# Performance work log

Hardware: AMD Instinct MI355X
Metric: run time of the kernel (lower is better)

## Reference

```python
import jax, jax.numpy as jnp
import numpy as np

B, S, I, C, N, V, O = 32, 256, 256, 512, 1024, 64, 256
EPS = 1e-12


def setup_inputs() -> dict:
    key = jax.random.key(0)
    ks = iter(jax.random.split(key, 40))

    def rn(shape, scale=0.05):
        return (jax.random.normal(next(ks), shape, jnp.float32) * scale)

    inp = {
        'x': jax.random.normal(next(ks), (B, S, I), jnp.float32),
        # LSTM controller (PyTorch gate order i,f,g,o)
        'lstm_Wih': rn((4 * C, I + V)), 'lstm_Whh': rn((4 * C, C)),
        'lstm_bih': rn((4 * C,)), 'lstm_bhh': rn((4 * C,)),
        # read head
        'r_key_W': rn((V, C)), 'r_key_b': rn((V,)),
        'r_str_W': rn((1, C)), 'r_str_b': rn((1,)),
        'r_gate_W': rn((1, C)), 'r_gate_b': rn((1,)),
        'r_shift_W': rn((3, C)), 'r_shift_b': rn((3,)),
        'r_gamma_W': rn((1, C)), 'r_gamma_b': rn((1,)),
        # write head (uses its own key/strength layers, plus erase/add)
        'w_key_W': rn((V, C)), 'w_key_b': rn((V,)),
        'w_str_W': rn((1, C)), 'w_str_b': rn((1,)),
        'w_erase_W': rn((V, C)), 'w_erase_b': rn((V,)),
        'w_add_W': rn((V, C)), 'w_add_b': rn((V,)),
        # output projection
        'out_W': rn((O, C + V)), 'out_b': rn((O,)),
    }
    return inp


def _lin(x, W, b):
    return x @ W.T + b


def _normalize(x, axis):
    n = jnp.linalg.norm(x, axis=axis, keepdims=True)
    return x / jnp.maximum(n, EPS)


def _content_addressing(key_vec, memory, strength):
    # key_vec: [B,V], memory: [B,N,V], strength: [B,1]
    kn = _normalize(key_vec, 1)
    mn = _normalize(memory, 2)
    sim = jnp.einsum('bv,bnv->bn', kn, mn)
    return jax.nn.softmax(strength * sim, axis=1)


def _ntm_forward(x, lstm_Wih, lstm_Whh, lstm_bih, lstm_bhh,
                 r_key_W, r_key_b, r_str_W, r_str_b, r_gate_W, r_gate_b,
                 r_shift_W, r_shift_b, r_gamma_W, r_gamma_b,
                 w_key_W, w_key_b, w_str_W, w_str_b,
                 w_erase_W, w_erase_b, w_add_W, w_add_b, out_W, out_b):
    b = x.shape[0]
    h0 = jnp.zeros((b, C), x.dtype)
    c0 = jnp.zeros((b, C), x.dtype)
    mem0 = jnp.zeros((b, N, V), x.dtype)
    rv0 = jnp.zeros((b, V), x.dtype)

    def step(carry, xt):
        h, c, memory, read_vec = carry
        # LSTM cell
        ci = jnp.concatenate([xt, read_vec], axis=1)          # [B, I+V]
        gates = _lin(ci, lstm_Wih, lstm_bih) + _lin(h, lstm_Whh, lstm_bhh)
        ig, fg, gg, og = jnp.split(gates, 4, axis=1)
        c = jax.nn.sigmoid(fg) * c + jax.nn.sigmoid(ig) * jnp.tanh(gg)
        h = jax.nn.sigmoid(og) * jnp.tanh(c)

        # read head
        key_r = jnp.tanh(_lin(h, r_key_W, r_key_b))
        str_r = jax.nn.softplus(_lin(h, r_str_W, r_str_b))
        gate = jax.nn.sigmoid(_lin(h, r_gate_W, r_gate_b))
        _shift = jax.nn.softmax(_lin(h, r_shift_W, r_shift_b), axis=1)  # computed but unused (as in source)
        gamma = 1.0 + jax.nn.softplus(_lin(h, r_gamma_W, r_gamma_b))
        cw = _content_addressing(key_r, memory, str_r)        # [B,N]
        sharp = cw ** gamma
        lw = sharp / jnp.sum(sharp, axis=1, keepdims=True)
        fw = gate * lw + (1.0 - gate) * cw
        read_vec = jnp.einsum('bn,bnv->bv', fw, memory)

        # write head (erase then add)
        key_w = jnp.tanh(_lin(h, w_key_W, w_key_b))
        str_w = jax.nn.softplus(_lin(h, w_str_W, w_str_b))
        ww = _content_addressing(key_w, memory, str_w)        # [B,N]
        erase = jax.nn.sigmoid(_lin(h, w_erase_W, w_erase_b))  # [B,V]
        add = jnp.tanh(_lin(h, w_add_W, w_add_b))              # [B,V]
        memory = memory * (1.0 - ww[:, :, None] * erase[:, None, :]) \
                 + ww[:, :, None] * add[:, None, :]

        out = _lin(jnp.concatenate([h, read_vec], axis=1), out_W, out_b)
        return (h, c, memory, read_vec), out

    (_, _, final_memory, _), outs = jax.lax.scan(
        step, (h0, c0, mem0, rv0), jnp.swapaxes(x, 0, 1))
    return jnp.swapaxes(outs, 0, 1), final_memory


def reference(x, lstm_Wih, lstm_Whh, lstm_bih, lstm_bhh,
              r_key_W, r_key_b, r_str_W, r_str_b, r_gate_W, r_gate_b,
              r_shift_W, r_shift_b, r_gamma_W, r_gamma_b,
              w_key_W, w_key_b, w_str_W, w_str_b,
              w_erase_W, w_erase_b, w_add_W, w_add_b, out_W, out_b):
    return _ntm_forward(x, lstm_Wih, lstm_Whh, lstm_bih, lstm_bhh,
                        r_key_W, r_key_b, r_str_W, r_str_b, r_gate_W, r_gate_b,
                        r_shift_W, r_shift_b, r_gamma_W, r_gamma_b,
                        w_key_W, w_key_b, w_str_W, w_str_b,
                        w_erase_W, w_erase_b, w_add_W, w_add_b, out_W, out_b)
```

## Files before the change

kernel.cpp:

```cpp
#include <hip/hip_runtime.h>

#define Bv 32
#define Sv 256
#define Iv 256
#define Cv 512
#define Nv 1024
#define Vv 64
#define Ov 256
#define NBLK 256
#define NTHR 256

#define CLAIM_I(x)   ((x)*8)
#define GAL_I(x,q)   (64 + ((x)*4+(q))*8)
#define XROOT_I(x)   (320 + (x)*8)
#define ZERO_BYTES   (640*4)
#define FBASE 1024
#define HBU(x,t1,bb)  (FBASE + (x)*2048 + (t1)*1024 + (bb)*256)
#define EGU(x,bb,k)   (FBASE + 16384 + (x)*2048 + (bb)*512 + (k)*64)
#define SUMPF(x,bb,k) (FBASE + 32768 + (x)*128 + (bb)*32 + (k)*4)
#define HPF(x,bb,r)   (FBASE + 33792 + (((x)*4+(bb))*32 + (r))*264)

struct KP {
  const float *x, *Wih, *Whh, *bih, *bhh;
  const float *rkW, *rkb, *rsW, *rsb, *rgW, *rgb, *rgammaW, *rgammab;
  const float *wkW, *wkb, *wsW, *wsb, *weW, *web, *waW, *wab;
  const float *outW, *outb;
  float *out;
  float *memout;
  float *ws;
};

typedef _Float16 half2v __attribute__((ext_vector_type(2)));
union HU { unsigned u; half2v h; };

__device__ inline float sigf(float x){ return 1.f/(1.f+expf(-x)); }
__device__ inline float softplusf(float x){ return fmaxf(x,0.f) + log1pf(expf(-fabsf(x))); }
__device__ inline unsigned packh(float a, float b){
  HU z; z.h = half2v{(_Float16)a, (_Float16)b}; return z.u;
}
__device__ inline float h2lo(unsigned u){ HU z; z.u = u; return (float)z.h.x; }
__device__ inline float h2hi(unsigned u){ HU z; z.u = u; return (float)z.h.y; }
__device__ inline float dot2(unsigned w, unsigned a, float acc){
  HU wu, au; wu.u = w; au.u = a;
  return __builtin_amdgcn_fdot2(wu.h, au.h, acc, false);
}

__device__ inline void stg_f(float* p, float v){
  asm volatile("global_store_dword %0, %1, off sc0" :: "v"(p), "v"(v) : "memory");
}
__device__ inline void stg_u(unsigned* p, unsigned v){
  asm volatile("global_store_dword %0, %1, off sc0" :: "v"(p), "v"(v) : "memory");
}
#define LDG4U(dst, addr) asm volatile("global_load_dwordx4 %0, %1, off sc0" : "=v"(dst) : "v"(addr) : "memory")
#define LDG4F(dst, addr) asm volatile("global_load_dwordx4 %0, %1, off sc0" : "=v"(dst) : "v"(addr) : "memory")
#define LDGU(dst, addr)  asm volatile("global_load_dword %0, %1, off sc0"  : "=v"(dst) : "v"(addr) : "memory")
#define LDGF(dst, addr)  asm volatile("global_load_dword %0, %1, off sc0"  : "=v"(dst) : "v"(addr) : "memory")
#define WAITV do { asm volatile("s_waitcnt vmcnt(0)" ::: "memory"); __builtin_amdgcn_sched_barrier(0); } while(0)

#define AADD(p,v) __hip_atomic_fetch_add((p),(v),__ATOMIC_RELAXED,__HIP_MEMORY_SCOPE_AGENT)
#define ALD(p)    __hip_atomic_load((p),__ATOMIC_RELAXED,__HIP_MEMORY_SCOPE_AGENT)

#define SPIN(cond_expr) do { unsigned sp = 0; \
  while (cond_expr){ __builtin_amdgcn_s_sleep(2); \
    if (((++sp)&1023u)==0u && (__builtin_amdgcn_s_memrealtime()-t0) > 300000000ULL) break; } } while(0)

__device__ inline float headact(int o, float s){
  if (o < 64)  return tanhf(s);
  if (o == 64) return softplusf(s);
  if (o == 65) return sigf(s);
  if (o == 66) return 1.f + softplusf(s);
  if (o < 131) return tanhf(s);
  if (o == 131) return softplusf(s);
  if (o < 196) return sigf(s);
  return tanhf(s);
}
__device__ inline void head_src(const KP& P, int o, const float** row, float* bias){
  if (o < 64)       { *row = P.rkW + o*Cv;        *bias = P.rkb[o]; }
  else if (o == 64) { *row = P.rsW;               *bias = P.rsb[0]; }
  else if (o == 65) { *row = P.rgW;               *bias = P.rgb[0]; }
  else if (o == 66) { *row = P.rgammaW;           *bias = P.rgammab[0]; }
  else if (o < 131) { *row = P.wkW + (o-67)*Cv;   *bias = P.wkb[o-67]; }
  else if (o == 131){ *row = P.wsW;               *bias = P.wsb[0]; }
  else if (o < 196) { *row = P.weW + (o-132)*Cv;  *bias = P.web[o-132]; }
  else              { *row = P.waW + (o-196)*Cv;  *bias = P.wab[o-196]; }
}

__global__ __launch_bounds__(NTHR) void ntm_kernel(KP P){
  __shared__ unsigned actL[4][420];
  __shared__ float memL[128][66];
  __shared__ float gbq[4][4][68];
  __shared__ float biasL[64];
  __shared__ float htmpf[16][5];
  __shared__ float headsL[264];
  __shared__ float pendE[64], pendA[64];
  __shared__ float knr[64], knw[64];
  __shared__ float scal[8];
  __shared__ float erL2[128], egL2[128], ewL[128];
  __shared__ float red[32][9];
  __shared__ float red2[2][4];
  __shared__ float sumS1[4][8][4];
  __shared__ float cEL[4], cGL[4];
  __shared__ float rvpE[4][64], rvpG[4][64];
  __shared__ float rvfinE[64], rvfinG[64];
  __shared__ int sXcd, sRank;

  const int tid = threadIdx.x;
  float* wsf = P.ws;
  unsigned* wsu = (unsigned*)P.ws;
  int* wsi = (int*)P.ws;
  const unsigned long long t0 = __builtin_amdgcn_s_memrealtime();

  if (tid == 0){
    unsigned xcc;
    asm volatile("s_getreg_b32 %0, hwreg(20, 0, 32)" : "=s"(xcc));
    int xc = (int)(xcc & 7u);
    int rk = AADD(&wsi[CLAIM_I(xc)], 1);
    sXcd = xc; sRank = rk & 31;
  }
  __syncthreads();
  const int xcd = sXcd, rank = sRank;
  const int bl_own = rank >> 3;
  const int rk8 = rank & 7;
  const int bglob = xcd*4 + bl_own;

  const int qw = tid >> 6;
  const int rw = tid & 63;
  const int grw = (rw>>4)*Cv + rank*16 + (rw&15);
  uint4 wreg[26];
  {
    #pragma unroll
    for (int jj = 0; jj < 26; ++jj){
      unsigned uu[4];
      #pragma unroll
      for (int c = 0; c < 4; ++c){
        int e = qw*208 + 8*jj + 2*c;
        float2 w2;
        if (e < 320) w2 = *(const float2*)(P.Wih + grw*320 + e);
        else         w2 = *(const float2*)(P.Whh + grw*512 + (e-320));
        uu[c] = packh(w2.x, w2.y);
      }
      wreg[jj].x = uu[0]; wreg[jj].y = uu[1]; wreg[jj].z = uu[2]; wreg[jj].w = uu[3];
    }
  }
  if (tid < 64){
    int gr = (tid>>4)*Cv + rank*16 + (tid&15);
    biasL[tid] = P.bih[gr] + P.bhh[gr];
  }
  float wA[16], wB[16], bA = 0.f, bB = 0.f;
  {
    const float* rowA; head_src(P, tid, &rowA, &bA);
    #pragma unroll
    for (int j = 0; j < 16; ++j) wA[j] = rowA[rank*16 + j];
    const float* rowB; head_src(P, 256 + (tid & 3), &rowB, &bB);
    #pragma unroll
    for (int j = 0; j < 16; ++j) wB[j] = rowB[rank*16 + j];
  }
  for (int idx = tid; idx < 128*66; idx += NTHR) ((float*)memL)[idx] = 0.f;
  __syncthreads();

  float cS = 0.f;
  int gs = 0;
  const int sbb = tid>>6, spart = tid&63;
  float4 xv;
  uint4 hq = {};
  xv = *(const float4*)(P.x + ((size_t)(xcd*4+sbb)*Sv + 0)*Iv + spart*4);

  for (int t = 0; t < Sv; ++t){
    if (t > 0){
      unsigned e0,e1,e2,e3,e4,e5,e6,e7,g0,g1,g2,g3,g4,g5,g6,g7;
      float4 sv = {0,0,0,0};
      int b2 = tid>>5, j = tid&31;
      if (tid < 128){
        const unsigned* eb = wsu + EGU(xcd,b2,0) + j;
        LDGU(e0,eb+0*64); LDGU(e1,eb+1*64); LDGU(e2,eb+2*64); LDGU(e3,eb+3*64);
        LDGU(e4,eb+4*64); LDGU(e5,eb+5*64); LDGU(e6,eb+6*64); LDGU(e7,eb+7*64);
        const unsigned* ggb = eb + 32;
        LDGU(g0,ggb+0*64); LDGU(g1,ggb+1*64); LDGU(g2,ggb+2*64); LDGU(g3,ggb+3*64);
        LDGU(g4,ggb+4*64); LDGU(g5,ggb+5*64); LDGU(g6,ggb+6*64); LDGU(g7,ggb+7*64);
      }
      if (tid < 32){ LDG4F(sv, wsf + SUMPF(xcd, tid>>3, tid&7)); }
      WAITV;
      actL[sbb][spart*2]   = packh(xv.x, xv.y);
      actL[sbb][spart*2+1] = packh(xv.z, xv.w);
      *(uint4*)&actL[sbb][160 + spart*4] = hq;
      if (tid < 32) *(float4*)&sumS1[tid>>3][tid&7][0] = sv;
      __syncthreads();
      if (tid < 4){
        float Se = 0.f, Sg = 0.f;
        #pragma unroll
        for (int k2 = 0; k2 < 8; ++k2){ Se += sumS1[tid][k2][0]; Sg += sumS1[tid][k2][1]; }
        float g = sumS1[tid][0][3];
        cEL[tid] = (1.f - g)/Se;
        cGL[tid] = g/Sg;
      }
      if (tid == 0){
        float Sw = 0.f;
        #pragma unroll
        for (int k2 = 0; k2 < 8; ++k2) Sw += sumS1[0][k2][2] + sumS1[1][k2][2] + sumS1[2][k2][2] + sumS1[3][k2][2];
        scal[6] = 0.f;
      }
      __syncthreads();
      if (tid == 0){
        float Sw = 0.f;
        #pragma unroll
        for (int k2 = 0; k2 < 8; ++k2) Sw += sumS1[bl_own][k2][2];
        scal[6] = Sw;
      }
      if (tid < 128){
        float Elo = h2lo(e0)+h2lo(e1)+h2lo(e2)+h2lo(e3)+h2lo(e4)+h2lo(e5)+h2lo(e6)+h2lo(e7);
        float Ehi = h2hi(e0)+h2hi(e1)+h2hi(e2)+h2hi(e3)+h2hi(e4)+h2hi(e5)+h2hi(e6)+h2hi(e7);
        float Glo = h2lo(g0)+h2lo(g1)+h2lo(g2)+h2lo(g3)+h2lo(g4)+h2lo(g5)+h2lo(g6)+h2lo(g7);
        float Ghi = h2hi(g0)+h2hi(g1)+h2hi(g2)+h2hi(g3)+h2hi(g4)+h2hi(g5)+h2hi(g6)+h2hi(g7);
        actL[b2][128 + j] = packh(cGL[b2]*Glo + cEL[b2]*Elo, cGL[b2]*Ghi + cEL[b2]*Ehi);
      }
      __syncthreads();
      {
        float rSw = 1.f/scal[6];
        #pragma unroll 4
        for (int e9 = 0; e9 < 32; ++e9){
          int flat = tid + e9*256;
          int r = flat >> 6, v2 = flat & 63;
          float ww = ewL[r]*rSw;
          memL[r][v2] = memL[r][v2]*(1.f - ww*pendE[v2]) + ww*pendA[v2];
        }
      }
    } else {
      actL[sbb][spart*2]   = packh(xv.x, xv.y);
      actL[sbb][spart*2+1] = packh(xv.z, xv.w);
      for (int idx = tid; idx < 4*288; idx += NTHR){
        int bb2 = idx/288, u = 128 + idx%288;
        actL[bb2][u] = 0u;
      }
    }
    __syncthreads();
    {
      const int base0 = qw*104;
      float a00=0.f,a01=0.f,a10=0.f,a11=0.f,a20=0.f,a21=0.f,a30=0.f,a31=0.f;
      #pragma unroll
      for (int jj = 0; jj < 26; ++jj){
        uint4 w = wreg[jj];
        uint4 v0 = *(const uint4*)&actL[0][base0+4*jj];
        uint4 v1 = *(const uint4*)&actL[1][base0+4*jj];
        uint4 v2 = *(const uint4*)&actL[2][base0+4*jj];
        uint4 v3 = *(const uint4*)&actL[3][base0+4*jj];
        a00=dot2(w.x,v0.x,a00); a01=dot2(w.y,v0.y,a01); a00=dot2(w.z,v0.z,a00); a01=dot2(w.w,v0.w,a01);
        a10=dot2(w.x,v1.x,a10); a11=dot2(w.y,v1.y,a11); a10=dot2(w.z,v1.z,a10); a11=dot2(w.w,v1.w,a11);
        a20=dot2(w.x,v2.x,a20); a21=dot2(w.y,v2.y,a21); a20=dot2(w.z,v2.z,a20); a21=dot2(w.w,v2.w,a21);
        a30=dot2(w.x,v3.x,a30); a31=dot2(w.y,v3.y,a31); a30=dot2(w.z,v3.z,a30); a31=dot2(w.w,v3.w,a31);
      }
      gbq[qw][0][rw] = a00+a01;
      gbq[qw][1][rw] = a10+a11;
      gbq[qw][2][rw] = a20+a21;
      gbq[qw][3][rw] = a30+a31;
    }
    __syncthreads();
    if (tid < 64){
      int j = tid>>2, bb = tid&3;
      float ig = biasL[j]    + gbq[0][bb][j]    + gbq[1][bb][j]    + gbq[2][bb][j]    + gbq[3][bb][j];
      float fg = biasL[16+j] + gbq[0][bb][16+j] + gbq[1][bb][16+j] + gbq[2][bb][16+j] + gbq[3][bb][16+j];
      float gg = biasL[32+j] + gbq[0][bb][32+j] + gbq[1][bb][32+j] + gbq[2][bb][32+j] + gbq[3][bb][32+j];
      float og = biasL[48+j] + gbq[0][bb][48+j] + gbq[1][bb][48+j] + gbq[2][bb][48+j] + gbq[3][bb][48+j];
      cS = sigf(fg)*cS + sigf(ig)*tanhf(gg);
      htmpf[j][bb] = sigf(og)*tanhf(cS);
    }
    __syncthreads();
    if (tid < 32){
      int pr = tid>>2, bb = tid&3;
      stg_u(wsu + HBU(xcd,t&1,bb) + rank*8 + pr, packh(htmpf[2*pr][bb], htmpf[2*pr+1][bb]));
    }
    {
      float p0=0.f,p1=0.f,p2=0.f,p3=0.f,q0=0.f,q1=0.f,q2=0.f,q3=0.f;
      #pragma unroll
      for (int j = 0; j < 16; ++j){
        float h0=htmpf[j][0], h1=htmpf[j][1], h2=htmpf[j][2], h3=htmpf[j][3];
        p0+=wA[j]*h0; p1+=wA[j]*h1; p2+=wA[j]*h2; p3+=wA[j]*h3;
        q0+=wB[j]*h0; q1+=wB[j]*h1; q2+=wB[j]*h2; q3+=wB[j]*h3;
      }
      stg_f(wsf + HPF(xcd,0,rank) + tid, p0);
      stg_f(wsf + HPF(xcd,1,rank) + tid, p1);
      stg_f(wsf + HPF(xcd,2,rank) + tid, p2);
      stg_f(wsf + HPF(xcd,3,rank) + tid, p3);
      if (tid < 4){
        int o2 = 256 + tid;
        stg_f(wsf + HPF(xcd,0,rank) + o2, q0);
        stg_f(wsf + HPF(xcd,1,rank) + o2, q1);
        stg_f(wsf + HPF(xcd,2,rank) + o2, q2);
        stg_f(wsf + HPF(xcd,3,rank) + o2, q3);
      }
    }
    WAITV;
    __syncthreads();
    if (tid == 0){
      int a = AADD(&wsi[GAL_I(xcd, rank>>3)], 1);
      if (a == 8*(gs+1) - 1) AADD(&wsi[XROOT_I(xcd)], 1);
    }
    if (t > 0){
      int oo = tid>>3, kc = tid&7;
      int o = rk8*32 + oo;
      const float* wrow = P.outW + o*576 + kc*72;
      const unsigned* ab = &actL[bl_own][0];
      float p = 0.f;
      if (kc < 7){
        int u0 = 160 + kc*36;
        #pragma unroll 9
        for (int i = 0; i < 36; ++i){
          unsigned u = ab[u0+i];
          p += h2lo(u)*wrow[2*i] + h2hi(u)*wrow[2*i+1];
        }
      } else {
        #pragma unroll
        for (int i = 0; i < 4; ++i){
          unsigned u = ab[412+i];
          p += h2lo(u)*wrow[2*i] + h2hi(u)*wrow[2*i+1];
        }
        #pragma unroll 8
        for (int i = 0; i < 32; ++i){
          unsigned u = ab[128+i];
          p += h2lo(u)*wrow[8+2*i] + h2hi(u)*wrow[9+2*i];
        }
      }
      red[oo][kc] = p;
      __syncthreads();
      if (tid < 32){
        int o2 = rk8*32 + tid;
        float s = P.outb[o2];
        #pragma unroll
        for (int k2 = 0; k2 < 8; ++k2) s += red[tid][k2];
        P.out[((size_t)bglob*Sv + (t-1))*Ov + o2] = s;
      }
    }
    if (tid == 0){ SPIN(ALD(&wsi[XROOT_I(xcd)]) < 4*(gs+1)); }
    __syncthreads();
    ++gs;

    {
      float s = bA, s2 = bB;
      #pragma unroll
      for (int half = 0; half < 2; ++half){
        const float* hb = wsf + HPF(xcd, bl_own, half*16);
        float av[16], bv[16];
        #pragma unroll
        for (int i = 0; i < 16; ++i){ LDGF(av[i], hb + i*264 + tid); }
        if (tid < 4){
          #pragma unroll
          for (int i = 0; i < 16; ++i){ LDGF(bv[i], hb + i*264 + 256 + tid); }
        }
        WAITV;
        #pragma unroll
        for (int i = 0; i < 16; ++i) s += av[i];
        if (tid < 4){
          #pragma unroll
          for (int i = 0; i < 16; ++i) s2 += bv[i];
        }
      }
      float hv = headact(tid, s);
      headsL[tid] = hv;
      if (tid >= 132 && tid < 196) pendE[tid-132] = hv;
      if (tid >= 196) pendA[tid-196] = hv;
      if (tid < 4){
        float hv2 = headact(256+tid, s2);
        headsL[256+tid] = hv2;
        pendA[60+tid] = hv2;
      }
    }
    __syncthreads();
    if (tid < 64){
      float kr = headsL[tid], kw = headsL[67+tid];
      float sr = kr*kr, sw2 = kw*kw;
      #pragma unroll
      for (int off = 32; off; off >>= 1){ sr += __shfl_xor(sr, off); sw2 += __shfl_xor(sw2, off); }
      knr[tid] = kr * (1.f/fmaxf(sqrtf(sr), 1e-12f));
      knw[tid] = kw * (1.f/fmaxf(sqrtf(sw2), 1e-12f));
    }
    __syncthreads();
    {
      float str_r = headsL[64], gamma = headsL[66], str_w = headsL[131];
      float er = 0.f, eg = 0.f, ew = 0.f;
      if (tid < 128){
        float dr = 0.f, dw = 0.f, nn = 0.f;
        #pragma unroll 8
        for (int v = 0; v < 64; ++v){
          float m = memL[tid][v];
          dr += m*knr[v]; dw += m*knw[v]; nn += m*m;
        }
        float innm = 1.f/fmaxf(sqrtf(nn), 1e-12f);
        float tr = str_r*(dr*innm - 1.f);
        er = expf(tr);
        eg = expf(gamma*tr);
        ew = expf(str_w*(dw*innm - 1.f));
        erL2[tid] = er; egL2[tid] = eg; ewL[tid] = ew;
      }
      float s0 = er, s1 = eg, s2 = ew;
      #pragma unroll
      for (int off = 32; off; off >>= 1){
        s0 += __shfl_xor(s0, off); s1 += __shfl_xor(s1, off); s2 += __shfl_xor(s2, off);
      }
      if ((tid & 63) == 0 && tid < 128){
        int wv = tid>>6; red2[wv][0] = s0; red2[wv][1] = s1; red2[wv][2] = s2;
      }
      __syncthreads();
      if (tid == 0){
        float* sp = wsf + SUMPF(xcd,bl_own,rk8);
        stg_f(sp+0, red2[0][0]+red2[1][0]);
        stg_f(sp+1, red2[0][1]+red2[1][1]);
        stg_f(sp+2, red2[0][2]+red2[1][2]);
        stg_f(sp+3, headsL[65]);
      }
    }
    {
      int v = tid & 63, cc = tid >> 6;
      float pE = 0.f, pG = 0.f;
      #pragma unroll 8
      for (int j = 0; j < 32; ++j){
        int r = cc*32 + j;
        float m = memL[r][v];
        pE += erL2[r]*m; pG += egL2[r]*m;
      }
      rvpE[cc][v] = pE; rvpG[cc][v] = pG;
    }
    __syncthreads();
    if (tid < 64){
      rvfinE[tid] = rvpE[0][tid]+rvpE[1][tid]+rvpE[2][tid]+rvpE[3][tid];
      rvfinG[tid] = rvpG[0][tid]+rvpG[1][tid]+rvpG[2][tid]+rvpG[3][tid];
    }
    __syncthreads();
    if (tid < 32)
      stg_u(wsu + EGU(xcd,bl_own,rk8) + tid, packh(rvfinE[2*tid], rvfinE[2*tid+1]));
    else if (tid < 64)
      stg_u(wsu + EGU(xcd,bl_own,rk8) + tid, packh(rvfinG[2*(tid-32)], rvfinG[2*(tid-32)+1]));
    WAITV;
    __syncthreads();
    if (tid == 0){
      int a = AADD(&wsi[GAL_I(xcd, rank>>3)], 1);
      if (a == 8*(gs+1) - 1) AADD(&wsi[XROOT_I(xcd)], 1);
    }
    {
      if (t + 1 < Sv)
        xv = *(const float4*)(P.x + ((size_t)(xcd*4+sbb)*Sv + (size_t)(t+1))*Iv + spart*4);
      LDG4U(hq, wsu + HBU(xcd, t&1, sbb) + spart*4);
    }
    if (tid == 0){ SPIN(ALD(&wsi[XROOT_I(xcd)]) < 4*(gs+1)); }
    __syncthreads();
    ++gs;
  }

  {
    unsigned e0,e1,e2,e3,e4,e5,e6,e7,g0,g1,g2,g3,g4,g5,g6,g7;
    float4 sv = {0,0,0,0};
    int b2 = tid>>5, j = tid&31;
    if (tid < 128){
      const unsigned* eb = wsu + EGU(xcd,b2,0) + j;
      LDGU(e0,eb+0*64); LDGU(e1,eb+1*64); LDGU(e2,eb+2*64); LDGU(e3,eb+3*64);
      LDGU(e4,eb+4*64); LDGU(e5,eb+5*64); LDGU(e6,eb+6*64); LDGU(e7,eb+7*64);
      const unsigned* ggb = eb + 32;
      LDGU(g0,ggb+0*64); LDGU(g1,ggb+1*64); LDGU(g2,ggb+2*64); LDGU(g3,ggb+3*64);
      LDGU(g4,ggb+4*64); LDGU(g5,ggb+5*64); LDGU(g6,ggb+6*64); LDGU(g7,ggb+7*64);
    }
    if (tid < 32){ LDG4F(sv, wsf + SUMPF(xcd, tid>>3, tid&7)); }
    WAITV;
    *(uint4*)&actL[sbb][160 + spart*4] = hq;
    if (tid < 32) *(float4*)&sumS1[tid>>3][tid&7][0] = sv;
    __syncthreads();
    if (tid < 4){
      float Se = 0.f, Sg = 0.f;
      #pragma unroll
      for (int k2 = 0; k2 < 8; ++k2){ Se += sumS1[tid][k2][0]; Sg += sumS1[tid][k2][1]; }
      float g = sumS1[tid][0][3];
      cEL[tid] = (1.f - g)/Se;
      cGL[tid] = g/Sg;
    }
    if (tid == 0){
      float Sw = 0.f;
      #pragma unroll
      for (int k2 = 0; k2 < 8; ++k2) Sw += sumS1[bl_own][k2][2];
      scal[6] = Sw;
    }
    __syncthreads();
    if (tid < 128){
      float Elo = h2lo(e0)+h2lo(e1)+h2lo(e2)+h2lo(e3)+h2lo(e4)+h2lo(e5)+h2lo(e6)+h2lo(e7);
      float Ehi = h2hi(e0)+h2hi(e1)+h2hi(e2)+h2hi(e3)+h2hi(e4)+h2hi(e5)+h2hi(e6)+h2hi(e7);
      float Glo = h2lo(g0)+h2lo(g1)+h2lo(g2)+h2lo(g3)+h2lo(g4)+h2lo(g5)+h2lo(g6)+h2lo(g7);
      float Ghi = h2hi(g0)+h2hi(g1)+h2hi(g2)+h2hi(g3)+h2hi(g4)+h2hi(g5)+h2hi(g6)+h2hi(g7);
      actL[b2][128 + j] = packh(cGL[b2]*Glo + cEL[b2]*Elo, cGL[b2]*Ghi + cEL[b2]*Ehi);
    }
    __syncthreads();
    {
      float rSw = 1.f/scal[6];
      #pragma unroll 4
      for (int e9 = 0; e9 < 32; ++e9){
        int flat = tid + e9*256;
        int r = flat >> 6, v2 = flat & 63;
        float ww = ewL[r]*rSw;
        memL[r][v2] = memL[r][v2]*(1.f - ww*pendE[v2]) + ww*pendA[v2];
      }
    }
    __syncthreads();
  }
  {
    int oo = tid>>3, kc = tid&7;
    int o = rk8*32 + oo;
    const float* wrow = P.outW + o*576 + kc*72;
    const unsigned* ab = &actL[bl_own][0];
    float p = 0.f;
    if (kc < 7){
      int u0 = 160 + kc*36;
      #pragma unroll 9
      for (int i = 0; i < 36; ++i){
        unsigned u = ab[u0+i];
        p += h2lo(u)*wrow[2*i] + h2hi(u)*wrow[2*i+1];
      }
    } else {
      #pragma unroll
      for (int i = 0; i < 4; ++i){
        unsigned u = ab[412+i];
        p += h2lo(u)*wrow[2*i] + h2hi(u)*wrow[2*i+1];
      }
      #pragma unroll 8
      for (int i = 0; i < 32; ++i){
        unsigned u = ab[128+i];
        p += h2lo(u)*wrow[8+2*i] + h2hi(u)*wrow[9+2*i];
      }
    }
    red[oo][kc] = p;
    __syncthreads();
    if (tid < 32){
      int o2 = rk8*32 + tid;
      float s = P.outb[o2];
      #pragma unroll
      for (int k2 = 0; k2 < 8; ++k2) s += red[tid][k2];
      P.out[((size_t)bglob*Sv + (Sv-1))*Ov + o2] = s;
    }
  }
  for (int e9 = 0; e9 < 32; ++e9){
    int flat = tid + e9*256;
    int r = flat >> 6, v2 = flat & 63;
    P.memout[((size_t)bglob*Nv + (size_t)rk8*128 + r)*Vv + v2] = memL[r][v2];
  }
}

extern "C" void kernel_launch(void* const* d_in, const int* in_sizes, int n_in,
                              void* d_out, int out_size, void* d_ws, size_t ws_size,
                              hipStream_t stream) {
  (void)in_sizes; (void)n_in; (void)out_size; (void)ws_size;
  KP p;
  p.x       = (const float*)d_in[0];
  p.Wih     = (const float*)d_in[1];
  p.Whh     = (const float*)d_in[2];
  p.bih     = (const float*)d_in[3];
  p.bhh     = (const float*)d_in[4];
  p.rkW     = (const float*)d_in[5];  p.rkb     = (const float*)d_in[6];
  p.rsW     = (const float*)d_in[7];  p.rsb     = (const float*)d_in[8];
  p.rgW     = (const float*)d_in[9];  p.rgb     = (const float*)d_in[10];
  p.rgammaW = (const float*)d_in[13]; p.rgammab = (const float*)d_in[14];
  p.wkW     = (const float*)d_in[15]; p.wkb     = (const float*)d_in[16];
  p.wsW     = (const float*)d_in[17]; p.wsb     = (const float*)d_in[18];
  p.weW     = (const float*)d_in[19]; p.web     = (const float*)d_in[20];
  p.waW     = (const float*)d_in[21]; p.wab     = (const float*)d_in[22];
  p.outW    = (const float*)d_in[23]; p.outb    = (const float*)d_in[24];
  p.out     = (float*)d_out;
  p.memout  = (float*)d_out + (size_t)Bv*Sv*Ov;
  p.ws      = (float*)d_ws;

  hipMemsetAsync(d_ws, 0, ZERO_BYTES, stream);
  hipLaunchKernelGGL(ntm_kernel, dim3(NBLK), dim3(NTHR), 0, stream, p);
}
```

Measured before the change: 3.971 ms.

## Pack head partial sums as fp16 pairs, transpose layout, overlap memory update with gate GEMV

Head-projection partials exchanged between blocks are now packed as fp16 pairs in a rank-contiguous layout. Each reader thread fetches all 32 rank partials for two outputs with eight 16-byte loads instead of many scalar strided loads. The memory erase/add update moves after the LSTM gate dot products, removing two barriers and a redundant reduction. The spin sleep interval is also shortened. Summing partials in fp16 reduces precision and may affect accuracy.

```diff
diff --git a/kernel.cpp b/kernel.cpp
--- a/kernel.cpp
+++ b/kernel.cpp
@@ -18,7 +18,7 @@
 #define HBU(x,t1,bb)  (FBASE + (x)*2048 + (t1)*1024 + (bb)*256)
 #define EGU(x,bb,k)   (FBASE + 16384 + (x)*2048 + (bb)*512 + (k)*64)
 #define SUMPF(x,bb,k) (FBASE + 32768 + (x)*128 + (bb)*32 + (k)*4)
-#define HPF(x,bb,r)   (FBASE + 33792 + (((x)*4+(bb))*32 + (r))*264)
+#define HPU(x,bb,m)   (FBASE + 33792 + (((x)*4+(bb))*132 + (m))*32)
 
 struct KP {
   const float *x, *Wih, *Whh, *bih, *bhh;
@@ -61,7 +61,7 @@
 #define ALD(p)    __hip_atomic_load((p),__ATOMIC_RELAXED,__HIP_MEMORY_SCOPE_AGENT)
 
 #define SPIN(cond_expr) do { unsigned sp = 0; \
-  while (cond_expr){ __builtin_amdgcn_s_sleep(2); \
+  while (cond_expr){ __builtin_amdgcn_s_sleep(1); \
     if (((++sp)&1023u)==0u && (__builtin_amdgcn_s_memrealtime()-t0) > 300000000ULL) break; } } while(0)
 
 __device__ inline float headact(int o, float s){
@@ -146,14 +146,22 @@
     int gr = (tid>>4)*Cv + rank*16 + (tid&15);
     biasL[tid] = P.bih[gr] + P.bhh[gr];
   }
-  float wA[16], wB[16], bA = 0.f, bB = 0.f;
+  float wA[16], wB[16];
   {
-    const float* rowA; head_src(P, tid, &rowA, &bA);
+    const float* rowA; float dummy;
+    head_src(P, tid, &rowA, &dummy);
     #pragma unroll
     for (int j = 0; j < 16; ++j) wA[j] = rowA[rank*16 + j];
-    const float* rowB; head_src(P, 256 + (tid & 3), &rowB, &bB);
+    const float* rowB;
+    head_src(P, 256 + (tid & 3), &rowB, &dummy);
     #pragma unroll
     for (int j = 0; j < 16; ++j) wB[j] = rowB[rank*16 + j];
+  }
+  float bLo = 0.f, bHi = 0.f;
+  if (tid < 130){
+    const float* rr2;
+    head_src(P, 2*tid,   &rr2, &bLo);
+    head_src(P, 2*tid+1, &rr2, &bHi);
   }
   for (int idx = tid; idx < 128*66; idx += NTHR) ((float*)memL)[idx] = 0.f;
   __syncthreads();
@@ -196,13 +204,6 @@
       if (tid == 0){
         float Sw = 0.f;
         #pragma unroll
-        for (int k2 = 0; k2 < 8; ++k2) Sw += sumS1[0][k2][2] + sumS1[1][k2][2] + sumS1[2][k2][2] + sumS1[3][k2][2];
-        scal[6] = 0.f;
-      }
-      __syncthreads();
-      if (tid == 0){
-        float Sw = 0.f;
-        #pragma unroll
         for (int k2 = 0; k2 < 8; ++k2) Sw += sumS1[bl_own][k2][2];
         scal[6] = Sw;
       }
@@ -212,17 +213,6 @@
         float Glo = h2lo(g0)+h2lo(g1)+h2lo(g2)+h2lo(g3)+h2lo(g4)+h2lo(g5)+h2lo(g6)+h2lo(g7);
         float Ghi = h2hi(g0)+h2hi(g1)+h2hi(g2)+h2hi(g3)+h2hi(g4)+h2hi(g5)+h2hi(g6)+h2hi(g7);
         actL[b2][128 + j] = packh(cGL[b2]*Glo + cEL[b2]*Elo, cGL[b2]*Ghi + cEL[b2]*Ehi);
-      }
-      __syncthreads();
-      {
-        float rSw = 1.f/scal[6];
-        #pragma unroll 4
-        for (int e9 = 0; e9 < 32; ++e9){
-          int flat = tid + e9*256;
-          int r = flat >> 6, v2 = flat & 63;
-          float ww = ewL[r]*rSw;
-          memL[r][v2] = memL[r][v2]*(1.f - ww*pendE[v2]) + ww*pendA[v2];
-        }
       }
     } else {
       actL[sbb][spart*2]   = packh(xv.x, xv.y);
@@ -252,6 +242,16 @@
       gbq[qw][1][rw] = a10+a11;
       gbq[qw][2][rw] = a20+a21;
       gbq[qw][3][rw] = a30+a31;
+      if (t > 0){
+        float rSw = 1.f/scal[6];
+        #pragma unroll 4
+        for (int e9 = 0; e9 < 32; ++e9){
+          int flat = tid + e9*256;
+          int r = flat >> 6, v2 = flat & 63;
+          float ww = ewL[r]*rSw;
+          memL[r][v2] = memL[r][v2]*(1.f - ww*pendE[v2]) + ww*pendA[v2];
+        }
+      }
     }
     __syncthreads();
     if (tid < 64){
@@ -276,16 +276,21 @@
         p0+=wA[j]*h0; p1+=wA[j]*h1; p2+=wA[j]*h2; p3+=wA[j]*h3;
         q0+=wB[j]*h0; q1+=wB[j]*h1; q2+=wB[j]*h2; q3+=wB[j]*h3;
       }
-      stg_f(wsf + HPF(xcd,0,rank) + tid, p0);
-      stg_f(wsf + HPF(xcd,1,rank) + tid, p1);
-      stg_f(wsf + HPF(xcd,2,rank) + tid, p2);
-      stg_f(wsf + HPF(xcd,3,rank) + tid, p3);
-      if (tid < 4){
-        int o2 = 256 + tid;
-        stg_f(wsf + HPF(xcd,0,rank) + o2, q0);
-        stg_f(wsf + HPF(xcd,1,rank) + o2, q1);
-        stg_f(wsf + HPF(xcd,2,rank) + o2, q2);
-        stg_f(wsf + HPF(xcd,3,rank) + o2, q3);
+      float o0 = __shfl_xor(p0,1), o1 = __shfl_xor(p1,1), o2 = __shfl_xor(p2,1), o3 = __shfl_xor(p3,1);
+      float r0 = __shfl_xor(q0,1), r1 = __shfl_xor(q1,1), r2 = __shfl_xor(q2,1), r3 = __shfl_xor(q3,1);
+      if ((tid & 1) == 0){
+        int m = tid >> 1;
+        stg_u(wsu + HPU(xcd,0,m) + rank, packh(p0,o0));
+        stg_u(wsu + HPU(xcd,1,m) + rank, packh(p1,o1));
+        stg_u(wsu + HPU(xcd,2,m) + rank, packh(p2,o2));
+        stg_u(wsu + HPU(xcd,3,m) + rank, packh(p3,o3));
+        if (tid < 4){
+          int m2 = 128 + (tid>>1);
+          stg_u(wsu + HPU(xcd,0,m2) + rank, packh(q0,r0));
+          stg_u(wsu + HPU(xcd,1,m2) + rank, packh(q1,r1));
+          stg_u(wsu + HPU(xcd,2,m2) + rank, packh(q2,r2));
+          stg_u(wsu + HPU(xcd,3,m2) + rank, packh(q3,r3));
+        }
       }
     }
     WAITV;
@@ -333,35 +338,25 @@
     __syncthreads();
     ++gs;
 
-    {
-      float s = bA, s2 = bB;
-      #pragma unroll
-      for (int half = 0; half < 2; ++half){
-        const float* hb = wsf + HPF(xcd, bl_own, half*16);
-        float av[16], bv[16];
-        #pragma unroll
-        for (int i = 0; i < 16; ++i){ LDGF(av[i], hb + i*264 + tid); }
-        if (tid < 4){
-          #pragma unroll
-          for (int i = 0; i < 16; ++i){ LDGF(bv[i], hb + i*264 + 256 + tid); }
-        }
-        WAITV;
-        #pragma unroll
-        for (int i = 0; i < 16; ++i) s += av[i];
-        if (tid < 4){
-          #pragma unroll
-          for (int i = 0; i < 16; ++i) s2 += bv[i];
-        }
-      }
-      float hv = headact(tid, s);
-      headsL[tid] = hv;
-      if (tid >= 132 && tid < 196) pendE[tid-132] = hv;
-      if (tid >= 196) pendA[tid-196] = hv;
-      if (tid < 4){
-        float hv2 = headact(256+tid, s2);
-        headsL[256+tid] = hv2;
-        pendA[60+tid] = hv2;
-      }
+    if (tid < 130){
+      const unsigned* hb = wsu + HPU(xcd, bl_own, tid);
+      uint4 v0,v1,v2,v3,v4,v5,v6,v7;
+      LDG4U(v0, hb+0);  LDG4U(v1, hb+4);  LDG4U(v2, hb+8);  LDG4U(v3, hb+12);
+      LDG4U(v4, hb+16); LDG4U(v5, hb+20); LDG4U(v6, hb+24); LDG4U(v7, hb+28);
+      WAITV;
+      float slo = bLo, shi = bHi;
+      #define ACC4(vv) do { \
+        slo += h2lo(vv.x)+h2lo(vv.y)+h2lo(vv.z)+h2lo(vv.w); \
+        shi += h2hi(vv.x)+h2hi(vv.y)+h2hi(vv.z)+h2hi(vv.w); } while(0)
+      ACC4(v0); ACC4(v1); ACC4(v2); ACC4(v3); ACC4(v4); ACC4(v5); ACC4(v6); ACC4(v7);
+      #undef ACC4
+      int oL = 2*tid, oH = 2*tid+1;
+      float hlo = headact(oL, slo), hhi = headact(oH, shi);
+      headsL[oL] = hlo; headsL[oH] = hhi;
+      if (oL >= 132 && oL < 196) pendE[oL-132] = hlo;
+      else if (oL >= 196) pendA[oL-196] = hlo;
+      if (oH >= 132 && oH < 196) pendE[oH-132] = hhi;
+      else if (oH >= 196) pendA[oH-196] = hhi;
     }
     __syncthreads();
     if (tid < 64){
```

Measured after the change: 4.220 ms. +6.3%, slower.
